# Kernel tuning notes

Hardware: AMD Instinct MI355X
Metric: run time of the kernel (lower is better)

Reference implementation:

```python
import jax, jax.numpy as jnp
import numpy as np

VOCAB, EMB, HID, T, B = 10000, 1500, 1500, 35, 64
FORGET_BIAS = 1.0

def setup_inputs() -> dict:
    key = jax.random.key(0)
    ks = jax.random.split(key, 8)
    s = 0.02
    return {
        'x': jax.random.randint(ks[0], (T, B), 0, VOCAB),
        'y': jax.random.randint(ks[1], (T, B), 0, VOCAB),
        'embedding': jax.random.normal(ks[2], (VOCAB, EMB), jnp.float32) * s,
        'W0': jax.random.normal(ks[3], (EMB + HID, 4 * HID), jnp.float32) * s,
        'b0': jnp.zeros((4 * HID,), jnp.float32),
        'W1': jax.random.normal(ks[4], (2 * HID, 4 * HID), jnp.float32) * s,
        'b1': jnp.zeros((4 * HID,), jnp.float32),
        'softmax_w': jax.random.normal(ks[5], (HID, VOCAB), jnp.float32) * 0.1,
        'softmax_b': jnp.zeros((VOCAB,), jnp.float32),
    }

def _lstm_step(c, h, x, W, b):
    # TF LSTMCell: z = [x, h] @ W + b; gate order i, j, f, o; forget_bias added to f
    z = jnp.concatenate([x, h], axis=-1) @ W + b
    i, j, f, o = jnp.split(z, 4, axis=-1)
    c_new = c * jax.nn.sigmoid(f + FORGET_BIAS) + jax.nn.sigmoid(i) * jnp.tanh(j)
    h_new = jnp.tanh(c_new) * jax.nn.sigmoid(o)
    return c_new, h_new

def reference(x, y, embedding, W0, b0, W1, b1, softmax_w, softmax_b):
    inputs = embedding[x]  # [T, B, EMB] (time_major)
    zeros = jnp.zeros((B, HID), inputs.dtype)
    init = (zeros, zeros, zeros, zeros)  # (c0, h0, c1, h1)

    def step(carry, xt):
        c0, h0, c1, h1 = carry
        c0, h0 = _lstm_step(c0, h0, xt, W0, b0)
        c1, h1 = _lstm_step(c1, h1, h0, W1, b1)
        return (c0, h0, c1, h1), h1

    _, outputs = jax.lax.scan(step, init, inputs)  # [T, B, HID]
    logits = outputs.reshape(-1, HID) @ softmax_w + softmax_b  # [T*B, VOCAB]
    logp = jax.nn.log_softmax(logits, axis=-1)
    tgt = y.reshape(-1)
    nll = -jnp.take_along_axis(logp, tgt[:, None], axis=-1)[:, 0]
    loss = jnp.sum(nll) / B  # sequence_loss_by_example with unit weights, / batch_size
    return loss
```

## Files before the change

### kernel.cpp

```cpp
#include <hip/hip_runtime.h>
#include <math.h>

#define TT 35
#define BB 64
#define EMB 1500
#define HID 1500
#define VOCAB 10000
#define KT 3072
#define KG 768
#define NCH 24
#define KLP 1504
#define NBLK 158
#define MROWS 2240
#define MPAD 2304
#define LBLK 94
#define FORGET_BIAS 1.0f

typedef __bf16 bf16x8 __attribute__((ext_vector_type(8)));
typedef float f32x4 __attribute__((ext_vector_type(4)));

__device__ __forceinline__ unsigned short f2bf(float f) {
    unsigned int u = __builtin_bit_cast(unsigned int, f);
    u += 0x7fffu + ((u >> 16) & 1u);
    return (unsigned short)(u >> 16);
}
__device__ __forceinline__ float sigmoidf_(float x) { return 1.0f / (1.0f + expf(-x)); }

#define GLOAD_LDS16(gp, lp) __builtin_amdgcn_global_load_lds( \
    (const __attribute__((address_space(1))) void*)(gp),      \
    (__attribute__((address_space(3))) void*)(lp), 16, 0, 0)

__global__ __launch_bounds__(256) void convT(const float* __restrict__ W,
                                             unsigned short* __restrict__ WT,
                                             int K, int N, int KP) {
    __shared__ float tile[32][33];
    int tx = threadIdx.x, ty = threadIdx.y;
    int n0 = blockIdx.x * 32, k0 = blockIdx.y * 32;
#pragma unroll
    for (int i = 0; i < 4; ++i) {
        int k = k0 + ty + 8 * i, n = n0 + tx;
        tile[ty + 8 * i][tx] = (k < K && n < N) ? W[(size_t)k * N + n] : 0.f;
    }
    __syncthreads();
#pragma unroll
    for (int i = 0; i < 4; ++i) {
        int n = n0 + ty + 8 * i, k = k0 + tx;
        if (n < N) WT[(size_t)n * KP + k] = f2bf(tile[tx][ty + 8 * i]);
    }
}

__global__ __launch_bounds__(256) void embed_kernel(const int* __restrict__ x,
                                                    const float* __restrict__ emb,
                                                    unsigned short* __restrict__ A0) {
    int tok = blockIdx.x;
    int v = x[tok];
    const float* src = emb + (size_t)v * EMB;
    unsigned short* dst = A0 + (size_t)tok * KT;
    for (int i = threadIdx.x; i < EMB; i += 256) dst[i] = f2bf(src[i]);
}

__global__ __launch_bounds__(1024) void lstm_pair(
        const unsigned short* __restrict__ A_0, const unsigned short* __restrict__ WT_0,
        const float* __restrict__ bias_0, float* __restrict__ cst_0,
        unsigned short* __restrict__ d1_0, int s1_0, unsigned short* __restrict__ d2_0, int s2_0,
        const unsigned short* __restrict__ A_1, const unsigned short* __restrict__ WT_1,
        const float* __restrict__ bias_1, float* __restrict__ cst_1,
        unsigned short* __restrict__ d1_1, int s1_1, unsigned short* __restrict__ d2_1, int s2_1) {
    __shared__ __align__(16) unsigned char smem[131072];

    const unsigned short* A;  const unsigned short* WT;
    const float* bias;        float* cst;
    unsigned short* d1; int s1; unsigned short* d2; int s2;
    int nb;
    if (blockIdx.x < LBLK) {
        if (!A_0) return;
        A = A_0; WT = WT_0; bias = bias_0; cst = cst_0;
        d1 = d1_0; s1 = s1_0; d2 = d2_0; s2 = s2_0;
        nb = blockIdx.x;
    } else {
        if (!A_1) return;
        A = A_1; WT = WT_1; bias = bias_1; cst = cst_1;
        d1 = d1_1; s1 = s1_1; d2 = d2_1; s2 = s2_1;
        nb = blockIdx.x - LBLK;
    }

    int tid = threadIdx.x;
    int wv = tid >> 6, lane = tid & 63;
    int mt = wv & 3, kg = wv >> 2;
    int quad = lane >> 4, l16 = lane & 15;
    int col = nb * 16 + l16;

    int rr = lane >> 2, p = lane & 3;
    int sp = p ^ (rr & 3) ^ ((rr >> 2) & 3);
    int kbase = kg * KG;
    int q0 = mt * 2, q1 = q0 + 1;
    const unsigned short* gp[2];
    int ldsoff[2];
#pragma unroll
    for (int ii = 0; ii < 2; ++ii) {
        int q = ii ? q1 : q0;
        if (q < 4) {
            gp[ii] = A + (size_t)(16 * q + rr) * KT + kbase + sp * 8;
        } else {
            int g = q - 4;
            int ci = nb * 16 + rr; if (ci > HID - 1) ci = HID - 1;
            gp[ii] = WT + (size_t)(g * HID + ci) * KT + kbase + sp * 8;
        }
        ldsoff[ii] = ((q >> 2) * 4 + kg) * 4096 + (q & 3) * 1024;
    }

    int swz = (quad ^ (l16 & 3) ^ ((l16 >> 2) & 3)) * 16;
    int aoff = (0 * 4 + kg) * 4096 + (mt * 16 + l16) * 64 + swz;
    int boff = (1 * 4 + kg) * 4096 + l16 * 64 + swz;

    f32x4 acc0 = {0.f,0.f,0.f,0.f}, acc1 = acc0, acc2 = acc0, acc3 = acc0;

#pragma unroll
    for (int ci = 0; ci < 3; ++ci) {
        GLOAD_LDS16(gp[0] + ci * 32, smem + ci * 32768 + ldsoff[0]);
        GLOAD_LDS16(gp[1] + ci * 32, smem + ci * 32768 + ldsoff[1]);
    }

    for (int c = 0; c < NCH; ++c) {
        asm volatile("s_waitcnt vmcnt(4)" ::: "memory");
        __builtin_amdgcn_sched_barrier(0);
        __builtin_amdgcn_s_barrier();
        int cs = (c + 3 < NCH) ? (c + 3) : (NCH - 1);
        int bs_ = (c + 3) & 3;
        GLOAD_LDS16(gp[0] + cs * 32, smem + bs_ * 32768 + ldsoff[0]);
        GLOAD_LDS16(gp[1] + cs * 32, smem + bs_ * 32768 + ldsoff[1]);
        const unsigned char* base = smem + (c & 3) * 32768;
        bf16x8 a  = *(const bf16x8*)(base + aoff);
        bf16x8 b0 = *(const bf16x8*)(base + boff);
        bf16x8 b1 = *(const bf16x8*)(base + boff + 1024);
        bf16x8 b2 = *(const bf16x8*)(base + boff + 2048);
        bf16x8 b3 = *(const bf16x8*)(base + boff + 3072);
        __builtin_amdgcn_s_setprio(1);
        acc0 = __builtin_amdgcn_mfma_f32_16x16x32_bf16(a, b0, acc0, 0, 0, 0);
        acc1 = __builtin_amdgcn_mfma_f32_16x16x32_bf16(a, b1, acc1, 0, 0, 0);
        acc2 = __builtin_amdgcn_mfma_f32_16x16x32_bf16(a, b2, acc2, 0, 0, 0);
        acc3 = __builtin_amdgcn_mfma_f32_16x16x32_bf16(a, b3, acc3, 0, 0, 0);
        __builtin_amdgcn_s_setprio(0);
    }
    asm volatile("s_waitcnt vmcnt(0)" ::: "memory");
    __builtin_amdgcn_sched_barrier(0);
    __syncthreads();

    float* red = (float*)smem;
    if (kg > 0) {
        int w = (kg - 1) * 4 + mt;
#pragma unroll
        for (int r = 0; r < 4; ++r) {
            red[(w * 64 + lane) * 16 + r]      = acc0[r];
            red[(w * 64 + lane) * 16 + 4 + r]  = acc1[r];
            red[(w * 64 + lane) * 16 + 8 + r]  = acc2[r];
            red[(w * 64 + lane) * 16 + 12 + r] = acc3[r];
        }
    }
    __syncthreads();
    if (kg == 0) {
#pragma unroll
        for (int k2 = 0; k2 < 3; ++k2) {
            int w = k2 * 4 + mt;
#pragma unroll
            for (int r = 0; r < 4; ++r) {
                acc0[r] += red[(w * 64 + lane) * 16 + r];
                acc1[r] += red[(w * 64 + lane) * 16 + 4 + r];
                acc2[r] += red[(w * 64 + lane) * 16 + 8 + r];
                acc3[r] += red[(w * 64 + lane) * 16 + 12 + r];
            }
        }
        if (col < HID) {
            float bi = bias[col], bj = bias[HID + col];
            float bf_ = bias[2 * HID + col], bo = bias[3 * HID + col];
#pragma unroll
            for (int r = 0; r < 4; ++r) {
                int row = mt * 16 + quad * 4 + r;
                float zi = acc0[r] + bi;
                float zj = acc1[r] + bj;
                float zf = acc2[r] + bf_;
                float zo = acc3[r] + bo;
                int ci = row * HID + col;
                float cn = cst[ci] * sigmoidf_(zf + FORGET_BIAS) + sigmoidf_(zi) * tanhf(zj);
                float hn = tanhf(cn) * sigmoidf_(zo);
                cst[ci] = cn;
                unsigned short hb = f2bf(hn);
                d1[(size_t)row * s1 + col] = hb;
                if (d2) d2[(size_t)row * s2 + col] = hb;
            }
        }
    }
}

__global__ __launch_bounds__(256) void logits_fold(const unsigned short* __restrict__ A,
                                                   const unsigned short* __restrict__ WT,
                                                   const float* __restrict__ sb,
                                                   const int* __restrict__ y,
                                                   float2* __restrict__ partials,
                                                   float* __restrict__ tgtlog) {
    __shared__ __align__(16) unsigned char smem[65536];

    int orig = blockIdx.x;
    int xcd = orig & 7, j = orig >> 3;
    int mb, bn;
    if (xcd < 7) { bn = xcd * 10 + j % 10; mb = j / 10; }
    else { if (j >= 162) return; bn = 70 + j % 9; mb = j / 9; }
    int n0 = bn * 128;

    int tid = threadIdx.x;
    int wv = tid >> 6, lane = tid & 63;
    int wr = wv >> 1, wc = wv & 1;
    int quad = lane >> 4, l16 = lane & 15;

    int rr = lane >> 2;
    int ks = (lane & 3) ^ (rr & 3) ^ ((rr >> 2) & 3);
    const unsigned short* gA[2]; const unsigned short* gB[2];
    int ldsA[2], ldsB[2];
#pragma unroll
    for (int i = 0; i < 2; ++i) {
        int r16 = wv * 2 + i;
        int ra = mb * 128 + r16 * 16 + rr;
        gA[i] = A + (size_t)ra * KLP + ks * 8;
        ldsA[i] = r16 * 1024;
        int rb = n0 + r16 * 16 + rr;
        if (rb > VOCAB - 1) rb = VOCAB - 1;
        gB[i] = WT + (size_t)rb * KLP + ks * 8;
        ldsB[i] = 8192 + r16 * 1024;
    }

    int sw16 = (quad ^ (l16 & 3) ^ ((l16 >> 2) & 3)) * 16;
    int aoff[4], boff[4];
#pragma unroll
    for (int f = 0; f < 4; ++f) {
        aoff[f] = (wr * 64 + f * 16 + l16) * 64 + sw16;
        boff[f] = 8192 + (wc * 64 + f * 16 + l16) * 64 + sw16;
    }

    f32x4 acc[4][4];
#pragma unroll
    for (int i = 0; i < 4; ++i)
#pragma unroll
        for (int jj = 0; jj < 4; ++jj) acc[i][jj] = (f32x4){0.f, 0.f, 0.f, 0.f};

    const int NCHL = KLP / 32;
#pragma unroll
    for (int ci = 0; ci < 3; ++ci)
#pragma unroll
        for (int i = 0; i < 2; ++i) {
            GLOAD_LDS16(gA[i] + ci * 32, smem + ci * 16384 + ldsA[i]);
            GLOAD_LDS16(gB[i] + ci * 32, smem + ci * 16384 + ldsB[i]);
        }
    for (int c = 0; c < NCHL; ++c) {
        asm volatile("s_waitcnt vmcnt(8)" ::: "memory");
        __builtin_amdgcn_sched_barrier(0);
        __builtin_amdgcn_s_barrier();
        int cs = (c + 3 < NCHL) ? (c + 3) : (NCHL - 1);
        int ob = ((c + 3) & 3) * 16384;
#pragma unroll
        for (int i = 0; i < 2; ++i) {
            GLOAD_LDS16(gA[i] + cs * 32, smem + ob + ldsA[i]);
            GLOAD_LDS16(gB[i] + cs * 32, smem + ob + ldsB[i]);
        }
        const unsigned char* base = smem + (c & 3) * 16384;
        bf16x8 a[4], b[4];
#pragma unroll
        for (int f = 0; f < 4; ++f) {
            a[f] = *(const bf16x8*)(base + aoff[f]);
            b[f] = *(const bf16x8*)(base + boff[f]);
        }
        __builtin_amdgcn_s_setprio(1);
#pragma unroll
        for (int ar = 0; ar < 4; ++ar)
#pragma unroll
            for (int cbv = 0; cbv < 4; ++cbv)
                acc[ar][cbv] = __builtin_amdgcn_mfma_f32_16x16x32_bf16(a[ar], b[cbv], acc[ar][cbv], 0, 0, 0);
        __builtin_amdgcn_s_setprio(0);
    }
    asm volatile("s_waitcnt vmcnt(0)" ::: "memory");
    __builtin_amdgcn_sched_barrier(0);
    __syncthreads();

    int colv[4]; float bs[4];
#pragma unroll
    for (int cbv = 0; cbv < 4; ++cbv) {
        int c = n0 + wc * 64 + cbv * 16 + l16;
        colv[cbv] = c;
        int cc = (c < VOCAB) ? c : (VOCAB - 1);
        bs[cbv] = sb[cc];
    }
    int nb2 = bn * 2 + wc;
#pragma unroll
    for (int ar = 0; ar < 4; ++ar) {
#pragma unroll
        for (int r2 = 0; r2 < 4; ++r2) {
            float v0 = acc[ar][0][r2] + bs[0];
            float v1 = acc[ar][1][r2] + bs[1];
            float v2 = acc[ar][2][r2] + bs[2];
            float v3 = acc[ar][3][r2] + bs[3];
            if (colv[0] >= VOCAB) v0 = -1e30f;
            if (colv[1] >= VOCAB) v1 = -1e30f;
            if (colv[2] >= VOCAB) v2 = -1e30f;
            if (colv[3] >= VOCAB) v3 = -1e30f;
            int row = mb * 128 + wr * 64 + ar * 16 + quad * 4 + r2;
            int t = y[row < MROWS ? row : 0];
            float tv = -1e30f;
            if (colv[0] == t) tv = v0;
            if (colv[1] == t) tv = v1;
            if (colv[2] == t) tv = v2;
            if (colv[3] == t) tv = v3;
            float mx = fmaxf(fmaxf(v0, v1), fmaxf(v2, v3));
#pragma unroll
            for (int d = 1; d < 16; d <<= 1) mx = fmaxf(mx, __shfl_xor(mx, d, 64));
            float sum = expf(v0 - mx) + expf(v1 - mx) + expf(v2 - mx) + expf(v3 - mx);
#pragma unroll
            for (int d = 1; d < 16; d <<= 1) sum += __shfl_xor(sum, d, 64);
#pragma unroll
            for (int d = 1; d < 16; d <<= 1) tv = fmaxf(tv, __shfl_xor(tv, d, 64));
            if (l16 == 0 && row < MROWS) {
                partials[(size_t)row * NBLK + nb2] = make_float2(mx, sum);
                if (tv > -5e29f) tgtlog[row] = tv;
            }
        }
    }
}

__global__ __launch_bounds__(64) void nll_reduce(const float2* __restrict__ partials,
                                                 const float* __restrict__ tgtlog,
                                                 float* __restrict__ nll) {
    int row = blockIdx.x;
    int lane = threadIdx.x;
    float2 loc[3];
    int cnt = 0;
    float m = -1e30f;
    for (int i = lane; i < NBLK; i += 64) {
        float2 p = partials[(size_t)row * NBLK + i];
        loc[cnt++] = p;
        m = fmaxf(m, p.x);
    }
#pragma unroll
    for (int d = 1; d < 64; d <<= 1) m = fmaxf(m, __shfl_xor(m, d, 64));
    float s = 0.f;
    for (int jj = 0; jj < cnt; ++jj) s += loc[jj].y * expf(loc[jj].x - m);
#pragma unroll
    for (int d = 1; d < 64; d <<= 1) s += __shfl_xor(s, d, 64);
    if (lane == 0) nll[row] = -(tgtlog[row] - m - logf(s));
}

__global__ __launch_bounds__(256) void loss_kernel(const float* __restrict__ nll,
                                                   float* __restrict__ out) {
    __shared__ float red[256];
    int tid = threadIdx.x;
    float s = 0.f;
    for (int i = tid; i < TT * BB; i += 256) s += nll[i];
    red[tid] = s; __syncthreads();
    for (int st = 128; st > 0; st >>= 1) { if (tid < st) red[tid] += red[tid + st]; __syncthreads(); }
    if (tid == 0) out[0] = red[0] / (float)BB;
}

extern "C" void kernel_launch(void* const* d_in, const int* in_sizes, int n_in,
                              void* d_out, int out_size, void* d_ws, size_t ws_size,
                              hipStream_t stream) {
    const int*   x   = (const int*)d_in[0];
    const int*   y   = (const int*)d_in[1];
    const float* emb = (const float*)d_in[2];
    const float* W0  = (const float*)d_in[3];
    const float* b0  = (const float*)d_in[4];
    const float* W1  = (const float*)d_in[5];
    const float* b1  = (const float*)d_in[6];
    const float* sw  = (const float*)d_in[7];
    const float* sb  = (const float*)d_in[8];
    float* out = (float*)d_out;

    char* p = (char*)d_ws;
    unsigned short* A0   = (unsigned short*)p; p += (size_t)TT * BB * KT * 2;
    unsigned short* A1   = (unsigned short*)p; p += (size_t)2 * BB * KT * 2;
    unsigned short* outs = (unsigned short*)p; p += (size_t)MPAD * KLP * 2;
    float* c0 = (float*)p; p += (size_t)BB * HID * 4;
    float* c1 = (float*)p; p += (size_t)BB * HID * 4;
    size_t zero_bytes = (size_t)(p - (char*)d_ws);
    unsigned short* WbT0 = (unsigned short*)p; p += (size_t)6000 * KT * 2;
    unsigned short* WbT1 = (unsigned short*)p; p += (size_t)6000 * KT * 2;
    unsigned short* swT  = (unsigned short*)p; p += (size_t)VOCAB * KLP * 2;
    float2* partials = (float2*)p; p += (size_t)TT * BB * NBLK * 8;
    float* tgtlog = (float*)p; p += (size_t)TT * BB * 4;
    float* nll    = (float*)p;

    hipMemsetAsync(d_ws, 0, zero_bytes, stream);

    dim3 cblk(32, 8);
    convT<<<dim3(188, 96), cblk, 0, stream>>>(W0, WbT0, 3000, 6000, KT);
    convT<<<dim3(188, 96), cblk, 0, stream>>>(W1, WbT1, 3000, 6000, KT);
    convT<<<dim3(313, 47), cblk, 0, stream>>>(sw, swT, HID, VOCAB, KLP);

    embed_kernel<<<TT * BB, 256, 0, stream>>>(x, emb, A0);

    for (int k = 0; k <= TT; ++k) {
        const unsigned short* A0t = (k < TT) ? A0 + (size_t)k * BB * KT : nullptr;
        unsigned short* d1_0 = A1 + (size_t)(k & 1) * BB * KT;
        unsigned short* d2_0 = (k < TT - 1) ? (A0 + (size_t)(k + 1) * BB * KT + EMB) : nullptr;

        const unsigned short* A1t = (k >= 1) ? A1 + (size_t)((k - 1) & 1) * BB * KT : nullptr;
        unsigned short* d1_1 = A1 + (size_t)(k & 1) * BB * KT + HID;
        unsigned short* d2_1 = (k >= 1) ? outs + (size_t)(k - 1) * BB * KLP : nullptr;

        lstm_pair<<<188, 1024, 0, stream>>>(A0t, WbT0, b0, c0, d1_0, KT, d2_0, KT,
                                            A1t, WbT1, b1, c1, d1_1, KT, d2_1, KLP);
    }

    logits_fold<<<1440, 256, 0, stream>>>(outs, swT, sb, y, partials, tgtlog);
    nll_reduce<<<TT * BB, 64, 0, stream>>>(partials, tgtlog, nll);
    loss_kernel<<<1, 256, 0, stream>>>(nll, out);
}
```

Baseline: 1.261 ms.

## Run each LSTM column block as one wave over full K; double-buffer logits GEMM

The LSTM step kernel goes from 16 waves per block, which split K four ways and reduced through LDS, to a single 64-thread wave per block. That wave computes all 64 batch rows by 4 gates over the full K=3072 with an 8-deep async global-to-LDS pipeline and no block barriers. The aim is to remove the cross-wave LDS reduction and the per-chunk barriers, at the cost of far less parallelism per block and a much longer serial MFMA chain per wave. The logits GEMM switches from a 4-stage vmcnt pipeline to a plain double buffer with __syncthreads, drops the s_setprio hints and simplifies the LDS swizzle, and uses half the shared memory.

```diff
diff --git a/kernel.cpp b/kernel.cpp
--- a/kernel.cpp
+++ b/kernel.cpp
@@ -7,8 +7,6 @@
 #define HID 1500
 #define VOCAB 10000
 #define KT 3072
-#define KG 768
-#define NCH 24
 #define KLP 1504
 #define NBLK 158
 #define MROWS 2240
@@ -59,127 +57,102 @@
     for (int i = threadIdx.x; i < EMB; i += 256) dst[i] = f2bf(src[i]);
 }
 
-__global__ __launch_bounds__(1024) void lstm_pair(
+__global__ __launch_bounds__(64) void lstm_pair(
         const unsigned short* __restrict__ A_0, const unsigned short* __restrict__ WT_0,
         const float* __restrict__ bias_0, float* __restrict__ cst_0,
         unsigned short* __restrict__ d1_0, int s1_0, unsigned short* __restrict__ d2_0, int s2_0,
         const unsigned short* __restrict__ A_1, const unsigned short* __restrict__ WT_1,
         const float* __restrict__ bias_1, float* __restrict__ cst_1,
         unsigned short* __restrict__ d1_1, int s1_1, unsigned short* __restrict__ d2_1, int s2_1) {
-    __shared__ __align__(16) unsigned char smem[131072];
+    __shared__ __align__(16) unsigned char smem[65536];
 
     const unsigned short* A;  const unsigned short* WT;
     const float* bias;        float* cst;
     unsigned short* d1; int s1; unsigned short* d2; int s2;
-    int nb;
+    int cb;
     if (blockIdx.x < LBLK) {
         if (!A_0) return;
         A = A_0; WT = WT_0; bias = bias_0; cst = cst_0;
         d1 = d1_0; s1 = s1_0; d2 = d2_0; s2 = s2_0;
-        nb = blockIdx.x;
+        cb = blockIdx.x;
     } else {
         if (!A_1) return;
         A = A_1; WT = WT_1; bias = bias_1; cst = cst_1;
         d1 = d1_1; s1 = s1_1; d2 = d2_1; s2 = s2_1;
-        nb = blockIdx.x - LBLK;
-    }
-
-    int tid = threadIdx.x;
-    int wv = tid >> 6, lane = tid & 63;
-    int mt = wv & 3, kg = wv >> 2;
+        cb = blockIdx.x - LBLK;
+    }
+
+    int lane = threadIdx.x;
     int quad = lane >> 4, l16 = lane & 15;
-    int col = nb * 16 + l16;
-
     int rr = lane >> 2, p = lane & 3;
     int sp = p ^ (rr & 3) ^ ((rr >> 2) & 3);
-    int kbase = kg * KG;
-    int q0 = mt * 2, q1 = q0 + 1;
-    const unsigned short* gp[2];
-    int ldsoff[2];
-#pragma unroll
-    for (int ii = 0; ii < 2; ++ii) {
-        int q = ii ? q1 : q0;
-        if (q < 4) {
-            gp[ii] = A + (size_t)(16 * q + rr) * KT + kbase + sp * 8;
-        } else {
-            int g = q - 4;
-            int ci = nb * 16 + rr; if (ci > HID - 1) ci = HID - 1;
-            gp[ii] = WT + (size_t)(g * HID + ci) * KT + kbase + sp * 8;
-        }
-        ldsoff[ii] = ((q >> 2) * 4 + kg) * 4096 + (q & 3) * 1024;
-    }
-
-    int swz = (quad ^ (l16 & 3) ^ ((l16 >> 2) & 3)) * 16;
-    int aoff = (0 * 4 + kg) * 4096 + (mt * 16 + l16) * 64 + swz;
-    int boff = (1 * 4 + kg) * 4096 + l16 * 64 + swz;
-
-    f32x4 acc0 = {0.f,0.f,0.f,0.f}, acc1 = acc0, acc2 = acc0, acc3 = acc0;
-
-#pragma unroll
-    for (int ci = 0; ci < 3; ++ci) {
-        GLOAD_LDS16(gp[0] + ci * 32, smem + ci * 32768 + ldsoff[0]);
-        GLOAD_LDS16(gp[1] + ci * 32, smem + ci * 32768 + ldsoff[1]);
-    }
-
-    for (int c = 0; c < NCH; ++c) {
-        asm volatile("s_waitcnt vmcnt(4)" ::: "memory");
+    int f16 = (l16 & 3) ^ ((l16 >> 2) & 3);
+
+    const unsigned short* gpA[4]; const unsigned short* gpB[4];
+#pragma unroll
+    for (int q = 0; q < 4; ++q) {
+        gpA[q] = A + (size_t)(16 * q + rr) * KT + sp * 8;
+        int ci = cb * 16 + rr; if (ci > HID - 1) ci = HID - 1;
+        gpB[q] = WT + (size_t)(q * HID + ci) * KT + sp * 8;
+    }
+    int ldsW = lane * 16;
+    int ro = l16 * 64 + ((quad ^ f16) * 16);
+
+    f32x4 acc[4][4];
+#pragma unroll
+    for (int i = 0; i < 4; ++i)
+#pragma unroll
+        for (int j = 0; j < 4; ++j) acc[i][j] = (f32x4){0.f, 0.f, 0.f, 0.f};
+
+#pragma unroll
+    for (int ci2 = 0; ci2 < 7; ++ci2)
+#pragma unroll
+        for (int q = 0; q < 4; ++q) {
+            GLOAD_LDS16(gpA[q] + ci2 * 32, smem + ci2 * 8192 + q * 1024 + ldsW);
+            GLOAD_LDS16(gpB[q] + ci2 * 32, smem + ci2 * 8192 + 4096 + q * 1024 + ldsW);
+        }
+
+    const int NCHF = KT / 32;
+    for (int c = 0; c < NCHF; ++c) {
+        asm volatile("s_waitcnt vmcnt(48)" ::: "memory");
         __builtin_amdgcn_sched_barrier(0);
-        __builtin_amdgcn_s_barrier();
-        int cs = (c + 3 < NCH) ? (c + 3) : (NCH - 1);
-        int bs_ = (c + 3) & 3;
-        GLOAD_LDS16(gp[0] + cs * 32, smem + bs_ * 32768 + ldsoff[0]);
-        GLOAD_LDS16(gp[1] + cs * 32, smem + bs_ * 32768 + ldsoff[1]);
-        const unsigned char* base = smem + (c & 3) * 32768;
-        bf16x8 a  = *(const bf16x8*)(base + aoff);
-        bf16x8 b0 = *(const bf16x8*)(base + boff);
-        bf16x8 b1 = *(const bf16x8*)(base + boff + 1024);
-        bf16x8 b2 = *(const bf16x8*)(base + boff + 2048);
-        bf16x8 b3 = *(const bf16x8*)(base + boff + 3072);
+        int cs = (c + 7 < NCHF) ? (c + 7) : (NCHF - 1);
+        int ob = ((c + 7) & 7) * 8192;
+#pragma unroll
+        for (int q = 0; q < 4; ++q) {
+            GLOAD_LDS16(gpA[q] + cs * 32, smem + ob + q * 1024 + ldsW);
+            GLOAD_LDS16(gpB[q] + cs * 32, smem + ob + 4096 + q * 1024 + ldsW);
+        }
+        const unsigned char* base = smem + (c & 7) * 8192;
+        bf16x8 a[4], b[4];
+#pragma unroll
+        for (int q = 0; q < 4; ++q) {
+            a[q] = *(const bf16x8*)(base + q * 1024 + ro);
+            b[q] = *(const bf16x8*)(base + 4096 + q * 1024 + ro);
+        }
         __builtin_amdgcn_s_setprio(1);
-        acc0 = __builtin_amdgcn_mfma_f32_16x16x32_bf16(a, b0, acc0, 0, 0, 0);
-        acc1 = __builtin_amdgcn_mfma_f32_16x16x32_bf16(a, b1, acc1, 0, 0, 0);
-        acc2 = __builtin_amdgcn_mfma_f32_16x16x32_bf16(a, b2, acc2, 0, 0, 0);
-        acc3 = __builtin_amdgcn_mfma_f32_16x16x32_bf16(a, b3, acc3, 0, 0, 0);
+#pragma unroll
+        for (int ar = 0; ar < 4; ++ar)
+#pragma unroll
+            for (int g = 0; g < 4; ++g)
+                acc[ar][g] = __builtin_amdgcn_mfma_f32_16x16x32_bf16(a[ar], b[g], acc[ar][g], 0, 0, 0);
         __builtin_amdgcn_s_setprio(0);
     }
     asm volatile("s_waitcnt vmcnt(0)" ::: "memory");
-    __builtin_amdgcn_sched_barrier(0);
-    __syncthreads();
-
-    float* red = (float*)smem;
-    if (kg > 0) {
-        int w = (kg - 1) * 4 + mt;
-#pragma unroll
-        for (int r = 0; r < 4; ++r) {
-            red[(w * 64 + lane) * 16 + r]      = acc0[r];
-            red[(w * 64 + lane) * 16 + 4 + r]  = acc1[r];
-            red[(w * 64 + lane) * 16 + 8 + r]  = acc2[r];
-            red[(w * 64 + lane) * 16 + 12 + r] = acc3[r];
-        }
-    }
-    __syncthreads();
-    if (kg == 0) {
-#pragma unroll
-        for (int k2 = 0; k2 < 3; ++k2) {
-            int w = k2 * 4 + mt;
+
+    int col = cb * 16 + l16;
+    if (col < HID) {
+        float bi = bias[col], bj = bias[HID + col];
+        float bf_ = bias[2 * HID + col], bo = bias[3 * HID + col];
+#pragma unroll
+        for (int ar = 0; ar < 4; ++ar)
 #pragma unroll
             for (int r = 0; r < 4; ++r) {
-                acc0[r] += red[(w * 64 + lane) * 16 + r];
-                acc1[r] += red[(w * 64 + lane) * 16 + 4 + r];
-                acc2[r] += red[(w * 64 + lane) * 16 + 8 + r];
-                acc3[r] += red[(w * 64 + lane) * 16 + 12 + r];
-            }
-        }
-        if (col < HID) {
-            float bi = bias[col], bj = bias[HID + col];
-            float bf_ = bias[2 * HID + col], bo = bias[3 * HID + col];
-#pragma unroll
-            for (int r = 0; r < 4; ++r) {
-                int row = mt * 16 + quad * 4 + r;
-                float zi = acc0[r] + bi;
-                float zj = acc1[r] + bj;
-                float zf = acc2[r] + bf_;
-                float zo = acc3[r] + bo;
+                int row = ar * 16 + quad * 4 + r;
+                float zi = acc[ar][0][r] + bi;
+                float zj = acc[ar][1][r] + bj;
+                float zf = acc[ar][2][r] + bf_;
+                float zo = acc[ar][3][r] + bo;
                 int ci = row * HID + col;
                 float cn = cst[ci] * sigmoidf_(zf + FORGET_BIAS) + sigmoidf_(zi) * tanhf(zj);
                 float hn = tanhf(cn) * sigmoidf_(zo);
@@ -188,7 +161,6 @@
                 d1[(size_t)row * s1 + col] = hb;
                 if (d2) d2[(size_t)row * s2 + col] = hb;
             }
-        }
     }
 }
 
@@ -198,7 +170,7 @@
                                                    const int* __restrict__ y,
                                                    float2* __restrict__ partials,
                                                    float* __restrict__ tgtlog) {
-    __shared__ __align__(16) unsigned char smem[65536];
+    __shared__ __align__(16) unsigned char smem[32768];
 
     int orig = blockIdx.x;
     int xcd = orig & 7, j = orig >> 3;
@@ -213,7 +185,7 @@
     int quad = lane >> 4, l16 = lane & 15;
 
     int rr = lane >> 2;
-    int ks = (lane & 3) ^ (rr & 3) ^ ((rr >> 2) & 3);
+    int ks = (lane & 3) ^ (rr & 3);
     const unsigned short* gA[2]; const unsigned short* gB[2];
     int ldsA[2], ldsB[2];
 #pragma unroll
@@ -228,7 +200,7 @@
         ldsB[i] = 8192 + r16 * 1024;
     }
 
-    int sw16 = (quad ^ (l16 & 3) ^ ((l16 >> 2) & 3)) * 16;
+    int sw16 = (quad ^ (l16 & 3)) * 16;
     int aoff[4], boff[4];
 #pragma unroll
     for (int f = 0; f < 4; ++f) {
@@ -242,43 +214,37 @@
 #pragma unroll
         for (int jj = 0; jj < 4; ++jj) acc[i][jj] = (f32x4){0.f, 0.f, 0.f, 0.f};
 
-    const int NCHL = KLP / 32;
-#pragma unroll
-    for (int ci = 0; ci < 3; ++ci)
-#pragma unroll
-        for (int i = 0; i < 2; ++i) {
-            GLOAD_LDS16(gA[i] + ci * 32, smem + ci * 16384 + ldsA[i]);
-            GLOAD_LDS16(gB[i] + ci * 32, smem + ci * 16384 + ldsB[i]);
-        }
-    for (int c = 0; c < NCHL; ++c) {
-        asm volatile("s_waitcnt vmcnt(8)" ::: "memory");
-        __builtin_amdgcn_sched_barrier(0);
-        __builtin_amdgcn_s_barrier();
-        int cs = (c + 3 < NCHL) ? (c + 3) : (NCHL - 1);
-        int ob = ((c + 3) & 3) * 16384;
-#pragma unroll
-        for (int i = 0; i < 2; ++i) {
-            GLOAD_LDS16(gA[i] + cs * 32, smem + ob + ldsA[i]);
-            GLOAD_LDS16(gB[i] + cs * 32, smem + ob + ldsB[i]);
-        }
-        const unsigned char* base = smem + (c & 3) * 16384;
+#pragma unroll
+    for (int i = 0; i < 2; ++i) {
+        GLOAD_LDS16(gA[i], smem + ldsA[i]);
+        GLOAD_LDS16(gB[i], smem + ldsB[i]);
+    }
+    __syncthreads();
+
+    for (int c = 0; c < KLP / 32; ++c) {
+        int buf = c & 1;
+        if (c + 1 < KLP / 32) {
+            int ob = (buf ^ 1) * 16384;
+#pragma unroll
+            for (int i = 0; i < 2; ++i) {
+                GLOAD_LDS16(gA[i] + (c + 1) * 32, smem + ob + ldsA[i]);
+                GLOAD_LDS16(gB[i] + (c + 1) * 32, smem + ob + ldsB[i]);
+            }
+        }
+        const unsigned char* base = smem + buf * 16384;
         bf16x8 a[4], b[4];
 #pragma unroll
         for (int f = 0; f < 4; ++f) {
             a[f] = *(const bf16x8*)(base + aoff[f]);
             b[f] = *(const bf16x8*)(base + boff[f]);
         }
-        __builtin_amdgcn_s_setprio(1);
 #pragma unroll
         for (int ar = 0; ar < 4; ++ar)
 #pragma unroll
             for (int cbv = 0; cbv < 4; ++cbv)
                 acc[ar][cbv] = __builtin_amdgcn_mfma_f32_16x16x32_bf16(a[ar], b[cbv], acc[ar][cbv], 0, 0, 0);
-        __builtin_amdgcn_s_setprio(0);
-    }
-    asm volatile("s_waitcnt vmcnt(0)" ::: "memory");
-    __builtin_amdgcn_sched_barrier(0);
-    __syncthreads();
+        __syncthreads();
+    }
 
     int colv[4]; float bs[4];
 #pragma unroll
@@ -403,8 +369,8 @@
         unsigned short* d1_1 = A1 + (size_t)(k & 1) * BB * KT + HID;
         unsigned short* d2_1 = (k >= 1) ? outs + (size_t)(k - 1) * BB * KLP : nullptr;
 
-        lstm_pair<<<188, 1024, 0, stream>>>(A0t, WbT0, b0, c0, d1_0, KT, d2_0, KT,
-                                            A1t, WbT1, b1, c1, d1_1, KT, d2_1, KLP);
+        lstm_pair<<<188, 64, 0, stream>>>(A0t, WbT0, b0, c0, d1_0, KT, d2_0, KT,
+                                          A1t, WbT1, b1, c1, d1_1, KT, d2_1, KLP);
     }
 
     logits_fold<<<1440, 256, 0, stream>>>(outs, swT, sb, y, partials, tgtlog);
```

Result: slower. 1.783 ms (+41.4%).

## Restructure LSTM and logits K-pipelines to coarser double buffering with simpler swizzle

Applied to the files above, without the earlier changes.

The LSTM step kernel moves from a 4-stage, one-chunk-per-iteration ring to double-buffered pairs of chunks. It waits for all loads at each barrier and then computes two chunks per iteration. The logits kernel drops from a 4-stage ring (64KB LDS) to a plain 2-stage double buffer (32KB LDS), removes the setprio hints, and simplifies the LDS XOR swizzle. The aim is to cut barrier count or LDS footprint so occupancy rises, at the cost of shallower prefetch and more exposed load latency. The simpler swizzle may also raise bank conflicts.

```diff
diff --git a/kernel.cpp b/kernel.cpp
--- a/kernel.cpp
+++ b/kernel.cpp
@@ -116,31 +116,40 @@
     f32x4 acc0 = {0.f,0.f,0.f,0.f}, acc1 = acc0, acc2 = acc0, acc3 = acc0;
 
 #pragma unroll
-    for (int ci = 0; ci < 3; ++ci) {
-        GLOAD_LDS16(gp[0] + ci * 32, smem + ci * 32768 + ldsoff[0]);
-        GLOAD_LDS16(gp[1] + ci * 32, smem + ci * 32768 + ldsoff[1]);
-    }
-
-    for (int c = 0; c < NCH; ++c) {
-        asm volatile("s_waitcnt vmcnt(4)" ::: "memory");
+    for (int s = 0; s < 2; ++s) {
+        GLOAD_LDS16(gp[0] + s * 32, smem + s * 32768 + ldsoff[0]);
+        GLOAD_LDS16(gp[1] + s * 32, smem + s * 32768 + ldsoff[1]);
+    }
+
+    const int NIT = NCH / 2;
+    for (int it = 0; it < NIT; ++it) {
+        asm volatile("s_waitcnt vmcnt(0)" ::: "memory");
         __builtin_amdgcn_sched_barrier(0);
         __builtin_amdgcn_s_barrier();
-        int cs = (c + 3 < NCH) ? (c + 3) : (NCH - 1);
-        int bs_ = (c + 3) & 3;
-        GLOAD_LDS16(gp[0] + cs * 32, smem + bs_ * 32768 + ldsoff[0]);
-        GLOAD_LDS16(gp[1] + cs * 32, smem + bs_ * 32768 + ldsoff[1]);
-        const unsigned char* base = smem + (c & 3) * 32768;
-        bf16x8 a  = *(const bf16x8*)(base + aoff);
-        bf16x8 b0 = *(const bf16x8*)(base + boff);
-        bf16x8 b1 = *(const bf16x8*)(base + boff + 1024);
-        bf16x8 b2 = *(const bf16x8*)(base + boff + 2048);
-        bf16x8 b3 = *(const bf16x8*)(base + boff + 3072);
-        __builtin_amdgcn_s_setprio(1);
-        acc0 = __builtin_amdgcn_mfma_f32_16x16x32_bf16(a, b0, acc0, 0, 0, 0);
-        acc1 = __builtin_amdgcn_mfma_f32_16x16x32_bf16(a, b1, acc1, 0, 0, 0);
-        acc2 = __builtin_amdgcn_mfma_f32_16x16x32_bf16(a, b2, acc2, 0, 0, 0);
-        acc3 = __builtin_amdgcn_mfma_f32_16x16x32_bf16(a, b3, acc3, 0, 0, 0);
-        __builtin_amdgcn_s_setprio(0);
+        if (it + 1 < NIT) {
+            int nb2 = ((it + 1) & 1) * 65536;
+#pragma unroll
+            for (int s = 0; s < 2; ++s) {
+                GLOAD_LDS16(gp[0] + (2 * (it + 1) + s) * 32, smem + nb2 + s * 32768 + ldsoff[0]);
+                GLOAD_LDS16(gp[1] + (2 * (it + 1) + s) * 32, smem + nb2 + s * 32768 + ldsoff[1]);
+            }
+        }
+        const unsigned char* base = smem + (it & 1) * 65536;
+#pragma unroll
+        for (int s = 0; s < 2; ++s) {
+            const unsigned char* bs2 = base + s * 32768;
+            bf16x8 a  = *(const bf16x8*)(bs2 + aoff);
+            bf16x8 b0 = *(const bf16x8*)(bs2 + boff);
+            bf16x8 b1 = *(const bf16x8*)(bs2 + boff + 1024);
+            bf16x8 b2 = *(const bf16x8*)(bs2 + boff + 2048);
+            bf16x8 b3 = *(const bf16x8*)(bs2 + boff + 3072);
+            __builtin_amdgcn_s_setprio(1);
+            acc0 = __builtin_amdgcn_mfma_f32_16x16x32_bf16(a, b0, acc0, 0, 0, 0);
+            acc1 = __builtin_amdgcn_mfma_f32_16x16x32_bf16(a, b1, acc1, 0, 0, 0);
+            acc2 = __builtin_amdgcn_mfma_f32_16x16x32_bf16(a, b2, acc2, 0, 0, 0);
+            acc3 = __builtin_amdgcn_mfma_f32_16x16x32_bf16(a, b3, acc3, 0, 0, 0);
+            __builtin_amdgcn_s_setprio(0);
+        }
     }
     asm volatile("s_waitcnt vmcnt(0)" ::: "memory");
     __builtin_amdgcn_sched_barrier(0);
@@ -198,7 +207,7 @@
                                                    const int* __restrict__ y,
                                                    float2* __restrict__ partials,
                                                    float* __restrict__ tgtlog) {
-    __shared__ __align__(16) unsigned char smem[65536];
+    __shared__ __align__(16) unsigned char smem[32768];
 
     int orig = blockIdx.x;
     int xcd = orig & 7, j = orig >> 3;
@@ -213,7 +222,7 @@
     int quad = lane >> 4, l16 = lane & 15;
 
     int rr = lane >> 2;
-    int ks = (lane & 3) ^ (rr & 3) ^ ((rr >> 2) & 3);
+    int ks = (lane & 3) ^ (rr & 3);
     const unsigned short* gA[2]; const unsigned short* gB[2];
     int ldsA[2], ldsB[2];
 #pragma unroll
@@ -228,7 +237,7 @@
         ldsB[i] = 8192 + r16 * 1024;
     }
 
-    int sw16 = (quad ^ (l16 & 3) ^ ((l16 >> 2) & 3)) * 16;
+    int sw16 = (quad ^ (l16 & 3)) * 16;
     int aoff[4], boff[4];
 #pragma unroll
     for (int f = 0; f < 4; ++f) {
@@ -242,43 +251,37 @@
 #pragma unroll
         for (int jj = 0; jj < 4; ++jj) acc[i][jj] = (f32x4){0.f, 0.f, 0.f, 0.f};
 
-    const int NCHL = KLP / 32;
-#pragma unroll
-    for (int ci = 0; ci < 3; ++ci)
-#pragma unroll
-        for (int i = 0; i < 2; ++i) {
-            GLOAD_LDS16(gA[i] + ci * 32, smem + ci * 16384 + ldsA[i]);
-            GLOAD_LDS16(gB[i] + ci * 32, smem + ci * 16384 + ldsB[i]);
-        }
-    for (int c = 0; c < NCHL; ++c) {
-        asm volatile("s_waitcnt vmcnt(8)" ::: "memory");
-        __builtin_amdgcn_sched_barrier(0);
-        __builtin_amdgcn_s_barrier();
-        int cs = (c + 3 < NCHL) ? (c + 3) : (NCHL - 1);
-        int ob = ((c + 3) & 3) * 16384;
-#pragma unroll
-        for (int i = 0; i < 2; ++i) {
-            GLOAD_LDS16(gA[i] + cs * 32, smem + ob + ldsA[i]);
-            GLOAD_LDS16(gB[i] + cs * 32, smem + ob + ldsB[i]);
-        }
-        const unsigned char* base = smem + (c & 3) * 16384;
+#pragma unroll
+    for (int i = 0; i < 2; ++i) {
+        GLOAD_LDS16(gA[i], smem + ldsA[i]);
+        GLOAD_LDS16(gB[i], smem + ldsB[i]);
+    }
+    __syncthreads();
+
+    for (int c = 0; c < KLP / 32; ++c) {
+        int buf = c & 1;
+        if (c + 1 < KLP / 32) {
+            int ob = (buf ^ 1) * 16384;
+#pragma unroll
+            for (int i = 0; i < 2; ++i) {
+                GLOAD_LDS16(gA[i] + (c + 1) * 32, smem + ob + ldsA[i]);
+                GLOAD_LDS16(gB[i] + (c + 1) * 32, smem + ob + ldsB[i]);
+            }
+        }
+        const unsigned char* base = smem + buf * 16384;
         bf16x8 a[4], b[4];
 #pragma unroll
         for (int f = 0; f < 4; ++f) {
             a[f] = *(const bf16x8*)(base + aoff[f]);
             b[f] = *(const bf16x8*)(base + boff[f]);
         }
-        __builtin_amdgcn_s_setprio(1);
 #pragma unroll
         for (int ar = 0; ar < 4; ++ar)
 #pragma unroll
             for (int cbv = 0; cbv < 4; ++cbv)
                 acc[ar][cbv] = __builtin_amdgcn_mfma_f32_16x16x32_bf16(a[ar], b[cbv], acc[ar][cbv], 0, 0, 0);
-        __builtin_amdgcn_s_setprio(0);
-    }
-    asm volatile("s_waitcnt vmcnt(0)" ::: "memory");
-    __builtin_amdgcn_sched_barrier(0);
-    __syncthreads();
+        __syncthreads();
+    }
 
     int colv[4]; float bs[4];
 #pragma unroll
```

New measurement: 1.324 ms. 5.0% more time.
